# Kernel tuning notes

Hardware: AMD Instinct MI355X
Metric: run time of the kernel (lower is better)

## Reference

```python
import jax, jax.numpy as jnp
import numpy as np

B, S, DIM = 2, 2048, 2048
H, DH = 16, 128
FF = 4 * DIM
EPS = 1e-5


def layer_norm(x, w, b, eps=EPS):
    m = jnp.mean(x, axis=-1, keepdims=True)
    v = jnp.mean(jnp.square(x - m), axis=-1, keepdims=True)
    return (x - m) * jax.lax.rsqrt(v + eps) * w + b


def apply_rotary(x, cos, sin):
    # x: [B, H, S, DH]; cos/sin: [S, DH//2]; complex multiply on (even, odd) pairs
    x2 = x.reshape(*x.shape[:-1], DH // 2, 2)
    x0, x1 = x2[..., 0], x2[..., 1]
    c = cos[None, None, :, :]
    s = sin[None, None, :, :]
    r0 = x0 * c - x1 * s
    r1 = x0 * s + x1 * c
    return jnp.stack([r0, r1], axis=-1).reshape(x.shape)


def setup_inputs() -> dict:
    key = jax.random.key(0)
    ks = jax.random.split(key, 16)
    sc = 0.02
    pos = jnp.arange(S, dtype=jnp.float32)[:, None]
    inv_freq = 1.0 / (10000.0 ** (jnp.arange(0, DH // 2, dtype=jnp.float32) / (DH // 2)))
    ang = pos * inv_freq[None, :]
    return {
        "hidden_states": jax.random.normal(ks[0], (B, S, DIM), jnp.float32),
        "freqs_cos": jnp.cos(ang),
        "freqs_sin": jnp.sin(ang),
        "wq": jax.random.normal(ks[1], (DIM, H * DH), jnp.float32) * sc,
        "wk": jax.random.normal(ks[2], (DIM, H * DH), jnp.float32) * sc,
        "wv": jax.random.normal(ks[3], (DIM, H * DH), jnp.float32) * sc,
        "nq_w": jnp.ones((DH,), jnp.float32),
        "nq_b": jnp.zeros((DH,), jnp.float32),
        "nk_w": jnp.ones((DH,), jnp.float32),
        "nk_b": jnp.zeros((DH,), jnp.float32),
        "wo": jax.random.normal(ks[4], (H * DH, DIM), jnp.float32) * sc,
        "bo": jnp.zeros((DIM,), jnp.float32),
        "ln1_w": jnp.ones((DIM,), jnp.float32),
        "ln1_b": jnp.zeros((DIM,), jnp.float32),
        "ln3_w": jnp.ones((DIM,), jnp.float32),
        "ln3_b": jnp.zeros((DIM,), jnp.float32),
        "w1": jax.random.normal(ks[5], (DIM, FF), jnp.float32) * sc,
        "b1": jnp.zeros((FF,), jnp.float32),
        "w2": jax.random.normal(ks[6], (FF, DIM), jnp.float32) * sc,
        "b2": jnp.zeros((DIM,), jnp.float32),
    }


def reference(hidden_states, freqs_cos, freqs_sin, wq, wk, wv, nq_w, nq_b, nk_w, nk_b,
              wo, bo, ln1_w, ln1_b, ln3_w, ln3_b, w1, b1, w2, b2):
    x = hidden_states
    # --- self-attention branch ---
    n = layer_norm(x, ln1_w, ln1_b)                       # [B,S,DIM]
    q = (n @ wq).reshape(B, S, H, DH)
    k = (n @ wk).reshape(B, S, H, DH)
    v = (n @ wv).reshape(B, S, H, DH)
    # per-head QK LayerNorm (norm over dim_head)
    q = layer_norm(q, nq_w, nq_b)
    k = layer_norm(k, nk_w, nk_b)
    q = q.transpose(0, 2, 1, 3)                            # [B,H,S,DH]
    k = k.transpose(0, 2, 1, 3)
    v = v.transpose(0, 2, 1, 3)
    q = apply_rotary(q, freqs_cos, freqs_sin)
    k = apply_rotary(k, freqs_cos, freqs_sin)
    scale = DH ** -0.5
    scores = jnp.einsum("bhqd,bhkd->bhqk", q, k) * scale   # [B,H,S,S]
    probs = jax.nn.softmax(scores, axis=-1)
    attn = jnp.einsum("bhqk,bhkd->bhqd", probs, v)         # [B,H,S,DH]
    attn = attn.transpose(0, 2, 1, 3).reshape(B, S, H * DH)
    x = x + (attn @ wo + bo)
    # --- feed-forward branch ---
    n = layer_norm(x, ln3_w, ln3_b)
    h = jax.nn.gelu(n @ w1 + b1, approximate=False)
    x = x + (h @ w2 + b2)
    return x
```

## Files before the change

### kernel.cpp

```cpp
#include <hip/hip_runtime.h>
#include <hip/hip_bf16.h>
#include <stdint.h>

typedef __hip_bfloat16 bf16;
typedef float v4f __attribute__((ext_vector_type(4)));
typedef short v8s __attribute__((ext_vector_type(8)));

#define DEV __device__ __forceinline__

DEV float b2f(bf16 x) { return __bfloat162float(x); }
DEV bf16 f2b(float x) { return __float2bfloat16(x); }

DEV void load4(const float* p, float* f) {
  float4 t = *(const float4*)p;
  f[0] = t.x; f[1] = t.y; f[2] = t.z; f[3] = t.w;
}
DEV void load4(const bf16* p, float* f) {
  union { uint2 u; bf16 h[4]; } t;
  t.u = *(const uint2*)p;
#pragma unroll
  for (int i = 0; i < 4; i++) f[i] = b2f(t.h[i]);
}
DEV void load8(const float* p, float* f) {
  float4 a = ((const float4*)p)[0], b = ((const float4*)p)[1];
  f[0] = a.x; f[1] = a.y; f[2] = a.z; f[3] = a.w;
  f[4] = b.x; f[5] = b.y; f[6] = b.z; f[7] = b.w;
}
DEV void load8(const bf16* p, float* f) {
  union { uint4 u; bf16 h[8]; } t;
  t.u = *(const uint4*)p;
#pragma unroll
  for (int i = 0; i < 8; i++) f[i] = b2f(t.h[i]);
}
DEV void store4(bf16* p, const float* f) {
  union { uint2 u; bf16 h[4]; } t;
#pragma unroll
  for (int i = 0; i < 4; i++) t.h[i] = f2b(f[i]);
  *(uint2*)p = t.u;
}
DEV void store4(float* p, const float* f) {
  *(float4*)p = make_float4(f[0], f[1], f[2], f[3]);
}

DEV void gld_lds16(const bf16* g, bf16* l) {
  auto gp = reinterpret_cast<const __attribute__((address_space(1))) uint32_t*>(
      reinterpret_cast<uintptr_t>(g));
  auto lp = reinterpret_cast<__attribute__((address_space(3))) uint32_t*>(
      reinterpret_cast<uintptr_t>(l));
  __builtin_amdgcn_global_load_lds(gp, lp, 16, 0, 0);
}

template <typename XT>
__global__ __launch_bounds__(256)
void ln2048_kernel(const XT* __restrict__ x, const float* __restrict__ w,
                   const float* __restrict__ b, bf16* __restrict__ y) {
  const int N = 2048;
  int row = blockIdx.x, tid = threadIdx.x;
  const XT* xr = x + (size_t)row * N;
  bf16* yr = y + (size_t)row * N;
  float f[8], s = 0.f, ss = 0.f;
  load8(xr + tid * 8, f);
#pragma unroll
  for (int i = 0; i < 8; i++) { s += f[i]; ss += f[i] * f[i]; }
#pragma unroll
  for (int off = 32; off >= 1; off >>= 1) {
    s  += __shfl_xor(s, off, 64);
    ss += __shfl_xor(ss, off, 64);
  }
  __shared__ float red0[4], red1[4];
  int wv = tid >> 6;
  if ((tid & 63) == 0) { red0[wv] = s; red1[wv] = ss; }
  __syncthreads();
  s  = red0[0] + red0[1] + red0[2] + red0[3];
  ss = red1[0] + red1[1] + red1[2] + red1[3];
  float mean = s * (1.f / N);
  float var  = ss * (1.f / N) - mean * mean;
  float inv  = rsqrtf(var + 1e-5f);
  float wf[8], bf_[8];
  load8(w + tid * 8, wf);
  load8(b + tid * 8, bf_);
  union { uint4 u; bf16 h[8]; } vo;
#pragma unroll
  for (int i = 0; i < 8; i++)
    vo.h[i] = f2b((f[i] - mean) * inv * wf[i] + bf_[i]);
  ((uint4*)yr)[tid] = vo.u;
}

__global__ __launch_bounds__(256)
void headln_rope_kernel(bf16* __restrict__ q, const float* __restrict__ w,
                        const float* __restrict__ b, const float* __restrict__ fcos,
                        const float* __restrict__ fsin) {
  int tid = threadIdx.x;
  int wv = tid >> 6, ln = tid & 63;
  int idx = blockIdx.x * 4 + wv;
  int row = idx >> 4, h = idx & 15;
  int srow = row & 2047;
  bf16* p = q + (size_t)row * 2048 + h * 128 + ln * 2;
  union { unsigned int u; bf16 h2[2]; } v;
  v.u = *(const unsigned int*)p;
  float x0 = b2f(v.h2[0]), x1 = b2f(v.h2[1]);
  float s = x0 + x1, ss = x0 * x0 + x1 * x1;
#pragma unroll
  for (int off = 32; off >= 1; off >>= 1) {
    s  += __shfl_xor(s, off, 64);
    ss += __shfl_xor(ss, off, 64);
  }
  float mean = s * (1.f / 128.f);
  float var  = ss * (1.f / 128.f) - mean * mean;
  float inv  = rsqrtf(var + 1e-5f);
  float w0 = w[ln * 2], w1 = w[ln * 2 + 1];
  float b0 = b[ln * 2], b1 = b[ln * 2 + 1];
  x0 = (x0 - mean) * inv * w0 + b0;
  x1 = (x1 - mean) * inv * w1 + b1;
  float c  = fcos[srow * 64 + ln];
  float sn = fsin[srow * 64 + ln];
  v.h2[0] = f2b(x0 * c - x1 * sn);
  v.h2[1] = f2b(x0 * sn + x1 * c);
  *(unsigned int*)p = v.u;
}

__global__ __launch_bounds__(256)
void convT_kernel(const float* __restrict__ src, bf16* __restrict__ dst,
                  int K, int N) {
  __shared__ float T[64][65];
  int n0 = blockIdx.x * 64, k0 = blockIdx.y * 64;
  int t = threadIdx.x;
  int tr = t >> 4, tc4 = (t & 15) * 4;
#pragma unroll
  for (int it = 0; it < 4; it++) {
    float4 v = *(const float4*)&src[(size_t)(k0 + tr + 16 * it) * N + n0 + tc4];
    T[tr + 16 * it][tc4 + 0] = v.x;
    T[tr + 16 * it][tc4 + 1] = v.y;
    T[tr + 16 * it][tc4 + 2] = v.z;
    T[tr + 16 * it][tc4 + 3] = v.w;
  }
  __syncthreads();
#pragma unroll
  for (int it = 0; it < 4; it++) {
    int n = tr + 16 * it;
    union { uint2 u; bf16 h[4]; } o;
#pragma unroll
    for (int c = 0; c < 4; c++) o.h[c] = f2b(T[tc4 + c][n]);
    *(uint2*)&dst[(size_t)(n0 + n) * K + k0 + tc4] = o.u;
  }
}

template <int EPI, typename RT, typename OT>
__global__ __launch_bounds__(256, 2)
void mfma_gemm_kernel(const bf16* __restrict__ A, const bf16* __restrict__ BT,
                      OT* __restrict__ C, const float* __restrict__ bias,
                      const RT* __restrict__ res, int M, int N, int K) {
  __shared__ __align__(16) bf16 As[128 * 32];
  __shared__ __align__(16) bf16 Bs[128 * 32];
  int tid = threadIdx.x;
  int lane = tid & 63, wave = tid >> 6;
  int wr = wave >> 1, wc = wave & 1;
  int m0 = blockIdx.y * 128, n0 = blockIdx.x * 128;

  int ls_row = lane >> 2;
  int ls_k   = (lane & 3) * 8;
  int t0 = 2 * wave, t1 = 2 * wave + 1;
  const bf16* gA0 = A  + (size_t)(m0 + 16 * t0 + ls_row) * K + ls_k;
  const bf16* gA1 = A  + (size_t)(m0 + 16 * t1 + ls_row) * K + ls_k;
  const bf16* gB0 = BT + (size_t)(n0 + 16 * t0 + ls_row) * K + ls_k;
  const bf16* gB1 = BT + (size_t)(n0 + 16 * t1 + ls_row) * K + ls_k;
  bf16* lA0 = As + t0 * 512;
  bf16* lA1 = As + t1 * 512;
  bf16* lB0 = Bs + t0 * 512;
  bf16* lB1 = Bs + t1 * 512;

  int fr = lane & 15, fk = (lane >> 4) * 8;
  const bf16* pA = As + (wr * 64 + fr) * 32 + fk;
  const bf16* pB = Bs + (wc * 64 + fr) * 32 + fk;

  v4f acc[4][4];
#pragma unroll
  for (int i = 0; i < 4; i++)
#pragma unroll
    for (int j = 0; j < 4; j++) acc[i][j] = (v4f){0.f, 0.f, 0.f, 0.f};

  for (int k0 = 0; k0 < K; k0 += 32) {
    __syncthreads();
    gld_lds16(gA0, lA0); gld_lds16(gA1, lA1);
    gld_lds16(gB0, lB0); gld_lds16(gB1, lB1);
    gA0 += 32; gA1 += 32; gB0 += 32; gB1 += 32;
    __syncthreads();
    v8s af[4], bfr[4];
#pragma unroll
    for (int i = 0; i < 4; i++) af[i]  = *(const v8s*)(pA + i * 16 * 32);
#pragma unroll
    for (int j = 0; j < 4; j++) bfr[j] = *(const v8s*)(pB + j * 16 * 32);
#pragma unroll
    for (int i = 0; i < 4; i++)
#pragma unroll
      for (int j = 0; j < 4; j++)
        acc[i][j] = __builtin_amdgcn_mfma_f32_16x16x32_bf16(af[i], bfr[j],
                                                            acc[i][j], 0, 0, 0);
  }

  int rq = (lane >> 4) * 4;
#pragma unroll
  for (int j = 0; j < 4; j++) {
    int n = n0 + wc * 64 + j * 16 + (lane & 15);
    float bb = (EPI >= 1) ? bias[n] : 0.f;
#pragma unroll
    for (int i = 0; i < 4; i++) {
#pragma unroll
      for (int r = 0; r < 4; r++) {
        int m = m0 + wr * 64 + i * 16 + rq + r;
        float val = acc[i][j][r] + bb;
        if (EPI == 2)
          val = 0.5f * val * (1.f + erff(val * 0.70710678118654752f));
        if (EPI == 1) {
          if constexpr (__is_same(RT, float)) val += res[(size_t)m * N + n];
          else                                val += b2f(res[(size_t)m * N + n]);
        }
        if constexpr (__is_same(OT, float)) C[(size_t)m * N + n] = val;
        else                                C[(size_t)m * N + n] = f2b(val);
      }
    }
  }
}

template <int EPI, typename RT, typename OT>
__global__ __launch_bounds__(256)
void gemm_kernel(const bf16* __restrict__ A, const float* __restrict__ Bm,
                 OT* __restrict__ C, const float* __restrict__ bias,
                 const RT* __restrict__ res, int M, int N, int K) {
  const int BK = 32;
  __shared__ __align__(16) float As[BK][68];
  __shared__ __align__(16) float Bs[BK][68];
  int tid = threadIdx.x;
  int bm = blockIdx.y, bn = blockIdx.x;
  int tx = tid & 15, ty = tid >> 4;
  int am = tid >> 2, ak8 = (tid & 3) * 8;
  int bkr = tid >> 3, bn8 = (tid & 7) * 8;
  const bf16* Aptr = A + (size_t)(bm * 64 + am) * K + ak8;
  const float* Bptr = Bm + (size_t)bkr * N + bn * 64 + bn8;
  float acc[4][4] = {};
  for (int k0 = 0; k0 < K; k0 += BK) {
    float av[8], bv[8];
    load8(Aptr, av);
    load8(Bptr, bv);
    __syncthreads();
#pragma unroll
    for (int j = 0; j < 8; j++) As[ak8 + j][am] = av[j];
#pragma unroll
    for (int j = 0; j < 8; j++) Bs[bkr][bn8 + j] = bv[j];
    __syncthreads();
    Aptr += BK;
    Bptr += (size_t)BK * N;
#pragma unroll 8
    for (int kk = 0; kk < BK; kk++) {
      float a0[4], b0[4];
      *(float4*)a0 = *(const float4*)&As[kk][ty * 4];
      *(float4*)b0 = *(const float4*)&Bs[kk][tx * 4];
#pragma unroll
      for (int i = 0; i < 4; i++)
#pragma unroll
        for (int j = 0; j < 4; j++)
          acc[i][j] += a0[i] * b0[j];
    }
  }
  int m0 = bm * 64 + ty * 4, n0 = bn * 64 + tx * 4;
#pragma unroll
  for (int i = 0; i < 4; i++) {
    float r4[4];
#pragma unroll
    for (int j = 0; j < 4; j++) r4[j] = acc[i][j];
    if (EPI >= 1) {
      float bb[4];
      load4(bias + n0, bb);
#pragma unroll
      for (int j = 0; j < 4; j++) r4[j] += bb[j];
    }
    if (EPI == 2) {
#pragma unroll
      for (int j = 0; j < 4; j++)
        r4[j] = 0.5f * r4[j] * (1.f + erff(r4[j] * 0.70710678118654752f));
    }
    if (EPI == 1) {
      float rr[4];
      load4(res + (size_t)(m0 + i) * N + n0, rr);
#pragma unroll
      for (int j = 0; j < 4; j++) r4[j] += rr[j];
    }
    store4(&C[(size_t)(m0 + i) * N + n0], r4);
  }
}

#define VSWZ(r) (((((r) >> 3) ^ (r)) & 7) << 4)

__global__ __launch_bounds__(256, 2)
void attn_kernel(const bf16* __restrict__ q, const bf16* __restrict__ k,
                 const bf16* __restrict__ v, bf16* __restrict__ o) {
  const int S = 2048, HD = 2048;
  __shared__ __align__(16) char smem[57856];
  char* Ks0 = smem;
  char* Ks1 = smem + 16384;
  char* VtB = smem + 32768;
  char* PB  = smem + 49152;
  float* Lp = (float*)(smem + 57344);

  int id = blockIdx.x;
  int swzb = (id & 7) * 128 + (id >> 3);
  int bh = swzb >> 5, qb = swzb & 31;
  int q0 = qb * 64;
  size_t base = (size_t)(bh >> 4) * S * HD + (size_t)(bh & 15) * 128;

  int tid = threadIdx.x;
  int lane = tid & 63, wave = tid >> 6;
  int wr = wave >> 1, wc = wave & 1;
  int fr = lane & 15, fg = lane >> 4;

  if (tid < 128) Lp[tid] = 0.f;

  union V4U { uint4 u; bf16 h[8]; };
  int vr0 = (tid & 15) * 4, vd0 = (tid >> 4) * 8;

#pragma unroll
  for (int t = 0; t < 4; t++) {
    int ti = wave * 4 + t;
    int r = ti * 4 + fg;
    int cb = (fr * 16) ^ ((r & 7) << 4);
    gld_lds16(q + base + (size_t)(q0 + r) * HD + (cb >> 1), (bf16*)Ks0 + ti * 512);
    gld_lds16(k + base + (size_t)r * HD + (cb >> 1), (bf16*)Ks1 + ti * 512);
  }
  V4U vA[4], vB[4];
#pragma unroll
  for (int j = 0; j < 4; j++)
    vA[j].u = *(const uint4*)&v[base + (size_t)(vr0 + j) * HD + vd0];
  __syncthreads();

  v8s qfrag[2][4];
#pragma unroll
  for (int i = 0; i < 2; i++)
#pragma unroll
    for (int kk = 0; kk < 4; kk++) {
      int row = wr * 32 + i * 16 + fr;
      int off = row * 256 + ((kk * 64 + fg * 16) ^ ((row & 7) << 4));
      qfrag[i][kk] = *(const v8s*)(Ks0 + off);
    }
  __syncthreads();

  v4f oacc[2][4];
#pragma unroll
  for (int i = 0; i < 2; i++)
#pragma unroll
    for (int j = 0; j < 4; j++) oacc[i][j] = (v4f){0.f, 0.f, 0.f, 0.f};

  const float scale = 0.08838834764831845f;

#define ATTN_TILE(KT, KCUR, KNXT, VCUR, VNXT, STAGE_NEXT)                     \
  {                                                                           \
    _Pragma("unroll")                                                         \
    for (int c = 0; c < 8; c++) {                                             \
      int d = vd0 + c;                                                        \
      union { uint2 u2; bf16 hh[4]; } pk;                                     \
      _Pragma("unroll")                                                       \
      for (int j = 0; j < 4; j++) pk.hh[j] = VCUR[j].h[c];                    \
      *(uint2*)(VtB + d * 128 + ((vr0 * 2) ^ VSWZ(d))) = pk.u2;               \
    }                                                                         \
    if (STAGE_NEXT) {                                                         \
      _Pragma("unroll")                                                       \
      for (int t = 0; t < 4; t++) {                                           \
        int ti = wave * 4 + t;                                                \
        int r = ti * 4 + fg;                                                  \
        int cb = (fr * 16) ^ ((r & 7) << 4);                                  \
        gld_lds16(k + base + (size_t)((KT) + 64 + r) * HD + (cb >> 1),        \
                  (bf16*)(KNXT) + ti * 512);                                  \
      }                                                                       \
      _Pragma("unroll")                                                       \
      for (int j = 0; j < 4; j++)                                             \
        VNXT[j].u =                                                           \
            *(const uint4*)&v[base + (size_t)((KT) + 64 + vr0 + j) * HD + vd0]; \
    }                                                                         \
    v4f sacc[2][2];                                                           \
    _Pragma("unroll")                                                         \
    for (int i = 0; i < 2; i++)                                               \
      _Pragma("unroll")                                                       \
      for (int j = 0; j < 2; j++) sacc[i][j] = (v4f){0.f, 0.f, 0.f, 0.f};     \
    __builtin_amdgcn_s_setprio(1);                                            \
    _Pragma("unroll")                                                         \
    for (int kk = 0; kk < 4; kk++) {                                          \
      v8s kf[2];                                                              \
      _Pragma("unroll")                                                       \
      for (int j = 0; j < 2; j++) {                                           \
        int row = wc * 32 + j * 16 + fr;                                      \
        int off = row * 256 + ((kk * 64 + fg * 16) ^ ((row & 7) << 4));       \
        kf[j] = *(const v8s*)((KCUR) + off);                                  \
      }                                                                       \
      _Pragma("unroll")                                                       \
      for (int i = 0; i < 2; i++)                                             \
        _Pragma("unroll")                                                     \
        for (int j = 0; j < 2; j++)                                           \
          sacc[i][j] = __builtin_amdgcn_mfma_f32_16x16x32_bf16(               \
              qfrag[i][kk], kf[j], sacc[i][j], 0, 0, 0);                      \
    }                                                                         \
    __builtin_amdgcn_s_setprio(0);                                            \
    _Pragma("unroll")                                                         \
    for (int i = 0; i < 2; i++)                                               \
      _Pragma("unroll")                                                       \
      for (int r = 0; r < 4; r++) {                                           \
        int qrow = wr * 32 + i * 16 + fg * 4 + r;                             \
        float e0 = __expf(sacc[i][0][r] * scale);                             \
        float e1 = __expf(sacc[i][1][r] * scale);                             \
        int sw = VSWZ(qrow);                                                  \
        int c0 = wc * 64 + fr * 2;                                            \
        *(bf16*)(PB + qrow * 128 + (c0 ^ sw)) = f2b(e0);                      \
        *(bf16*)(PB + qrow * 128 + ((c0 + 32) ^ sw)) = f2b(e1);               \
        float s_ = e0 + e1;                                                   \
        s_ += __shfl_xor(s_, 1, 64);                                          \
        s_ += __shfl_xor(s_, 2, 64);                                          \
        s_ += __shfl_xor(s_, 4, 64);                                          \
        s_ += __shfl_xor(s_, 8, 64);                                          \
        if (fr == 0) Lp[wc * 64 + qrow] += s_;                                \
      }                                                                       \
    __syncthreads();                                                          \
    __builtin_amdgcn_s_setprio(1);                                            \
    _Pragma("unroll")                                                         \
    for (int kk2 = 0; kk2 < 2; kk2++) {                                       \
      v8s pf[2], vf[4];                                                       \
      _Pragma("unroll")                                                       \
      for (int i = 0; i < 2; i++) {                                           \
        int row = wr * 32 + i * 16 + fr;                                      \
        int off = row * 128 + ((kk2 * 64 + fg * 16) ^ VSWZ(row));             \
        pf[i] = *(const v8s*)(PB + off);                                      \
      }                                                                       \
      _Pragma("unroll")                                                       \
      for (int j = 0; j < 4; j++) {                                           \
        int row = wc * 64 + j * 16 + fr;                                      \
        int off = row * 128 + ((kk2 * 64 + fg * 16) ^ VSWZ(row));             \
        vf[j] = *(const v8s*)(VtB + off);                                     \
      }                                                                       \
      _Pragma("unroll")                                                       \
      for (int i = 0; i < 2; i++)                                             \
        _Pragma("unroll")                                                     \
        for (int j = 0; j < 4; j++)                                           \
          oacc[i][j] = __builtin_amdgcn_mfma_f32_16x16x32_bf16(               \
              pf[i], vf[j], oacc[i][j], 0, 0, 0);                             \
    }                                                                         \
    __builtin_amdgcn_s_setprio(0);                                            \
    __syncthreads();                                                          \
  }

  for (int tp = 0; tp < 16; tp++) {
    int kt = tp * 128;
    ATTN_TILE(kt, Ks1, Ks0, vA, vB, true);
    ATTN_TILE(kt + 64, Ks0, Ks1, vB, vA, (tp < 15));
  }
#undef ATTN_TILE

#pragma unroll
  for (int i = 0; i < 2; i++)
#pragma unroll
    for (int r = 0; r < 4; r++) {
      int qrow = wr * 32 + i * 16 + fg * 4 + r;
      float linv = 1.f / (Lp[qrow] + Lp[64 + qrow]);
#pragma unroll
      for (int j = 0; j < 4; j++) {
        int d = wc * 64 + j * 16 + fr;
        o[base + (size_t)(q0 + qrow) * HD + d] = f2b(oacc[i][j][r] * linv);
      }
    }
}

extern "C" void kernel_launch(void* const* d_in, const int* in_sizes, int n_in,
                              void* d_out, int out_size, void* d_ws, size_t ws_size,
                              hipStream_t stream) {
  (void)in_sizes; (void)n_in; (void)out_size;
  const float* x    = (const float*)d_in[0];
  const float* fcos = (const float*)d_in[1];
  const float* fsin = (const float*)d_in[2];
  const float* wq   = (const float*)d_in[3];
  const float* wk   = (const float*)d_in[4];
  const float* wv   = (const float*)d_in[5];
  const float* nqw  = (const float*)d_in[6];
  const float* nqb  = (const float*)d_in[7];
  const float* nkw  = (const float*)d_in[8];
  const float* nkb  = (const float*)d_in[9];
  const float* wo   = (const float*)d_in[10];
  const float* bo   = (const float*)d_in[11];
  const float* ln1w = (const float*)d_in[12];
  const float* ln1b = (const float*)d_in[13];
  const float* ln3w = (const float*)d_in[14];
  const float* ln3b = (const float*)d_in[15];
  const float* w1   = (const float*)d_in[16];
  const float* b1   = (const float*)d_in[17];
  const float* w2   = (const float*)d_in[18];
  const float* b2   = (const float*)d_in[19];
  float* out = (float*)d_out;

  const size_t SEG = (size_t)4096 * 2048;
  bf16* base = (bf16*)d_ws;
  bf16* q        = base + 0 * SEG;
  bf16* k        = base + 1 * SEG;
  bf16* v        = base + 2 * SEG;
  bf16* n1       = base + 3 * SEG;
  bf16* attn_out = base + 3 * SEG;
  bf16* x2       = base + 4 * SEG;
  bf16* n3       = base + 5 * SEG;
  bf16* h        = base + 0 * SEG;

  dim3 blk(256);
  ln2048_kernel<float><<<4096, blk, 0, stream>>>(x, ln1w, ln1b, n1);

  bool mfma_path = ws_size >= (size_t)128 * 1024 * 1024;
  if (mfma_path) {
    bf16* W = base + 6 * SEG;
    bf16* wqT = W;
    bf16* wkT = W + 4 * 1024 * 1024;
    bf16* wvT = W + 8 * 1024 * 1024;
    bf16* woT = W;
    bf16* w1T = W;
    bf16* w2T = W;

    dim3 cg22(32, 32);
    dim3 g16(16, 32);
    dim3 g64(64, 32);

    convT_kernel<<<cg22, blk, 0, stream>>>(wq, wqT, 2048, 2048);
    convT_kernel<<<cg22, blk, 0, stream>>>(wk, wkT, 2048, 2048);
    convT_kernel<<<cg22, blk, 0, stream>>>(wv, wvT, 2048, 2048);
    mfma_gemm_kernel<0, float, bf16><<<g16, blk, 0, stream>>>(n1, wqT, q, nullptr, nullptr, 4096, 2048, 2048);
    mfma_gemm_kernel<0, float, bf16><<<g16, blk, 0, stream>>>(n1, wkT, k, nullptr, nullptr, 4096, 2048, 2048);
    mfma_gemm_kernel<0, float, bf16><<<g16, blk, 0, stream>>>(n1, wvT, v, nullptr, nullptr, 4096, 2048, 2048);
    headln_rope_kernel<<<16384, blk, 0, stream>>>(q, nqw, nqb, fcos, fsin);
    headln_rope_kernel<<<16384, blk, 0, stream>>>(k, nkw, nkb, fcos, fsin);
    attn_kernel<<<1024, blk, 0, stream>>>(q, k, v, attn_out);
    convT_kernel<<<cg22, blk, 0, stream>>>(wo, woT, 2048, 2048);
    mfma_gemm_kernel<1, float, bf16><<<g16, blk, 0, stream>>>(attn_out, woT, x2, bo, x, 4096, 2048, 2048);
    ln2048_kernel<bf16><<<4096, blk, 0, stream>>>(x2, ln3w, ln3b, n3);
    convT_kernel<<<dim3(128, 32), blk, 0, stream>>>(w1, w1T, 2048, 8192);
    mfma_gemm_kernel<2, float, bf16><<<g64, blk, 0, stream>>>(n3, w1T, h, b1, nullptr, 4096, 8192, 2048);
    convT_kernel<<<dim3(32, 128), blk, 0, stream>>>(w2, w2T, 8192, 2048);
    mfma_gemm_kernel<1, bf16, float><<<g16, blk, 0, stream>>>(h, w2T, out, b2, x2, 4096, 2048, 8192);
  } else {
    dim3 g2048(32, 64), g8192(128, 64);
    gemm_kernel<0, float, bf16><<<g2048, blk, 0, stream>>>(n1, wq, q, nullptr, nullptr, 4096, 2048, 2048);
    gemm_kernel<0, float, bf16><<<g2048, blk, 0, stream>>>(n1, wk, k, nullptr, nullptr, 4096, 2048, 2048);
    gemm_kernel<0, float, bf16><<<g2048, blk, 0, stream>>>(n1, wv, v, nullptr, nullptr, 4096, 2048, 2048);
    headln_rope_kernel<<<16384, blk, 0, stream>>>(q, nqw, nqb, fcos, fsin);
    headln_rope_kernel<<<16384, blk, 0, stream>>>(k, nkw, nkb, fcos, fsin);
    attn_kernel<<<1024, blk, 0, stream>>>(q, k, v, attn_out);
    gemm_kernel<1, float, bf16><<<g2048, blk, 0, stream>>>(attn_out, wo, x2, bo, x, 4096, 2048, 2048);
    ln2048_kernel<bf16><<<4096, blk, 0, stream>>>(x2, ln3w, ln3b, n3);
    gemm_kernel<2, float, bf16><<<g8192, blk, 0, stream>>>(n3, w1, h, b1, nullptr, 4096, 8192, 2048);
    gemm_kernel<1, bf16, float><<<g2048, blk, 0, stream>>>(h, w2, out, b2, x2, 4096, 2048, 8192);
  }
}
```

Baseline: 1.026 ms.

## Fuse QKV GEMMs, swizzle GEMM block order, and enlarge attention query tile

Replaces the three Q/K/V projection GEMMs with one launch over a concatenated N=6144, scattering output columns into separate segments through a new ldc/segment-stride epilogue. This relies on wqT/wkT/wvT and q/k/v being laid out contiguously. Adds an XCD-aware block-index swizzle to the MFMA GEMM. Doubles the attention query tile from 64 to 128 rows per block, so K/V are loaded half as often, at the cost of more registers and more LDS.

```diff
diff --git a/kernel.cpp b/kernel.cpp
--- a/kernel.cpp
+++ b/kernel.cpp
@@ -149,13 +149,20 @@
 __global__ __launch_bounds__(256, 2)
 void mfma_gemm_kernel(const bf16* __restrict__ A, const bf16* __restrict__ BT,
                       OT* __restrict__ C, const float* __restrict__ bias,
-                      const RT* __restrict__ res, int M, int N, int K) {
+                      const RT* __restrict__ res, int M, int N, int K,
+                      int ldc_log2, size_t seg_stride) {
   __shared__ __align__(16) bf16 As[128 * 32];
   __shared__ __align__(16) bf16 Bs[128 * 32];
   int tid = threadIdx.x;
   int lane = tid & 63, wave = tid >> 6;
   int wr = wave >> 1, wc = wave & 1;
-  int m0 = blockIdx.y * 128, n0 = blockIdx.x * 128;
+
+  int nbx = gridDim.x;
+  int bid = blockIdx.y * nbx + blockIdx.x;
+  int nwg = nbx * gridDim.y;
+  int cpx = nwg >> 3;
+  int swz = (bid & 7) * cpx + (bid >> 3);
+  int m0 = (swz / nbx) * 128, n0 = (swz % nbx) * 128;
 
   int ls_row = lane >> 2;
   int ls_k   = (lane & 3) * 8;
@@ -199,10 +206,12 @@
   }
 
   int rq = (lane >> 4) * 4;
+  int ldm = 1 << ldc_log2;
 #pragma unroll
   for (int j = 0; j < 4; j++) {
     int n = n0 + wc * 64 + j * 16 + (lane & 15);
     float bb = (EPI >= 1) ? bias[n] : 0.f;
+    size_t cseg = (size_t)(n >> ldc_log2) * seg_stride + (n & (ldm - 1));
 #pragma unroll
     for (int i = 0; i < 4; i++) {
 #pragma unroll
@@ -215,8 +224,9 @@
           if constexpr (__is_same(RT, float)) val += res[(size_t)m * N + n];
           else                                val += b2f(res[(size_t)m * N + n]);
         }
-        if constexpr (__is_same(OT, float)) C[(size_t)m * N + n] = val;
-        else                                C[(size_t)m * N + n] = f2b(val);
+        size_t cix = cseg + ((size_t)m << ldc_log2);
+        if constexpr (__is_same(OT, float)) C[cix] = val;
+        else                                C[cix] = f2b(val);
       }
     }
   }
@@ -295,17 +305,17 @@
 void attn_kernel(const bf16* __restrict__ q, const bf16* __restrict__ k,
                  const bf16* __restrict__ v, bf16* __restrict__ o) {
   const int S = 2048, HD = 2048;
-  __shared__ __align__(16) char smem[57856];
+  __shared__ __align__(16) char smem[66560];
   char* Ks0 = smem;
   char* Ks1 = smem + 16384;
   char* VtB = smem + 32768;
   char* PB  = smem + 49152;
-  float* Lp = (float*)(smem + 57344);
+  float* Lp = (float*)(smem + 65536);
 
   int id = blockIdx.x;
-  int swzb = (id & 7) * 128 + (id >> 3);
-  int bh = swzb >> 5, qb = swzb & 31;
-  int q0 = qb * 64;
+  int swzb = (id & 7) * 64 + (id >> 3);
+  int bh = swzb >> 4, qb = swzb & 15;
+  int q0 = qb * 128;
   size_t base = (size_t)(bh >> 4) * S * HD + (size_t)(bh & 15) * 128;
 
   int tid = threadIdx.x;
@@ -313,39 +323,51 @@
   int wr = wave >> 1, wc = wave & 1;
   int fr = lane & 15, fg = lane >> 4;
 
-  if (tid < 128) Lp[tid] = 0.f;
+  Lp[tid] = 0.f;
 
   union V4U { uint4 u; bf16 h[8]; };
   int vr0 = (tid & 15) * 4, vd0 = (tid >> 4) * 8;
+
+#pragma unroll
+  for (int t = 0; t < 8; t++) {
+    int ti = wave * 8 + t;
+    int r = ti * 4 + fg;
+    int cb = (fr * 16) ^ ((r & 7) << 4);
+    bf16* dst = (bf16*)(ti < 16 ? Ks0 : Ks1) + (ti & 15) * 512;
+    gld_lds16(q + base + (size_t)(q0 + r) * HD + (cb >> 1), dst);
+  }
+  V4U vA[4], vB[4];
+#pragma unroll
+  for (int j = 0; j < 4; j++)
+    vA[j].u = *(const uint4*)&v[base + (size_t)(vr0 + j) * HD + vd0];
+  __syncthreads();
+
+  v8s qfrag[4][4];
+  {
+    const char* qbuf = wr ? Ks1 : Ks0;
+#pragma unroll
+    for (int i = 0; i < 4; i++)
+#pragma unroll
+      for (int kk = 0; kk < 4; kk++) {
+        int rb = i * 16 + fr;
+        int off = rb * 256 + ((kk * 64 + fg * 16) ^ ((rb & 7) << 4));
+        qfrag[i][kk] = *(const v8s*)(qbuf + off);
+      }
+  }
+  __syncthreads();
 
 #pragma unroll
   for (int t = 0; t < 4; t++) {
     int ti = wave * 4 + t;
     int r = ti * 4 + fg;
     int cb = (fr * 16) ^ ((r & 7) << 4);
-    gld_lds16(q + base + (size_t)(q0 + r) * HD + (cb >> 1), (bf16*)Ks0 + ti * 512);
-    gld_lds16(k + base + (size_t)r * HD + (cb >> 1), (bf16*)Ks1 + ti * 512);
-  }
-  V4U vA[4], vB[4];
-#pragma unroll
-  for (int j = 0; j < 4; j++)
-    vA[j].u = *(const uint4*)&v[base + (size_t)(vr0 + j) * HD + vd0];
+    gld_lds16(k + base + (size_t)r * HD + (cb >> 1), (bf16*)Ks0 + ti * 512);
+  }
   __syncthreads();
 
-  v8s qfrag[2][4];
-#pragma unroll
-  for (int i = 0; i < 2; i++)
-#pragma unroll
-    for (int kk = 0; kk < 4; kk++) {
-      int row = wr * 32 + i * 16 + fr;
-      int off = row * 256 + ((kk * 64 + fg * 16) ^ ((row & 7) << 4));
-      qfrag[i][kk] = *(const v8s*)(Ks0 + off);
-    }
-  __syncthreads();
-
-  v4f oacc[2][4];
-#pragma unroll
-  for (int i = 0; i < 2; i++)
+  v4f oacc[4][4];
+#pragma unroll
+  for (int i = 0; i < 4; i++)
 #pragma unroll
     for (int j = 0; j < 4; j++) oacc[i][j] = (v4f){0.f, 0.f, 0.f, 0.f};
 
@@ -375,9 +397,9 @@
         VNXT[j].u =                                                           \
             *(const uint4*)&v[base + (size_t)((KT) + 64 + vr0 + j) * HD + vd0]; \
     }                                                                         \
-    v4f sacc[2][2];                                                           \
+    v4f sacc[4][2];                                                           \
     _Pragma("unroll")                                                         \
-    for (int i = 0; i < 2; i++)                                               \
+    for (int i = 0; i < 4; i++)                                               \
       _Pragma("unroll")                                                       \
       for (int j = 0; j < 2; j++) sacc[i][j] = (v4f){0.f, 0.f, 0.f, 0.f};     \
     __builtin_amdgcn_s_setprio(1);                                            \
@@ -391,7 +413,7 @@
         kf[j] = *(const v8s*)((KCUR) + off);                                  \
       }                                                                       \
       _Pragma("unroll")                                                       \
-      for (int i = 0; i < 2; i++)                                             \
+      for (int i = 0; i < 4; i++)                                             \
         _Pragma("unroll")                                                     \
         for (int j = 0; j < 2; j++)                                           \
           sacc[i][j] = __builtin_amdgcn_mfma_f32_16x16x32_bf16(               \
@@ -399,10 +421,10 @@
     }                                                                         \
     __builtin_amdgcn_s_setprio(0);                                            \
     _Pragma("unroll")                                                         \
-    for (int i = 0; i < 2; i++)                                               \
+    for (int i = 0; i < 4; i++)                                               \
       _Pragma("unroll")                                                       \
       for (int r = 0; r < 4; r++) {                                           \
-        int qrow = wr * 32 + i * 16 + fg * 4 + r;                             \
+        int qrow = wr * 64 + i * 16 + fg * 4 + r;                             \
         float e0 = __expf(sacc[i][0][r] * scale);                             \
         float e1 = __expf(sacc[i][1][r] * scale);                             \
         int sw = VSWZ(qrow);                                                  \
@@ -414,16 +436,16 @@
         s_ += __shfl_xor(s_, 2, 64);                                          \
         s_ += __shfl_xor(s_, 4, 64);                                          \
         s_ += __shfl_xor(s_, 8, 64);                                          \
-        if (fr == 0) Lp[wc * 64 + qrow] += s_;                                \
+        if (fr == 0) Lp[wc * 128 + qrow] += s_;                               \
       }                                                                       \
     __syncthreads();                                                          \
     __builtin_amdgcn_s_setprio(1);                                            \
     _Pragma("unroll")                                                         \
     for (int kk2 = 0; kk2 < 2; kk2++) {                                       \
-      v8s pf[2], vf[4];                                                       \
-      _Pragma("unroll")                                                       \
-      for (int i = 0; i < 2; i++) {                                           \
-        int row = wr * 32 + i * 16 + fr;                                      \
+      v8s pf[4], vf[4];                                                       \
+      _Pragma("unroll")                                                       \
+      for (int i = 0; i < 4; i++) {                                           \
+        int row = wr * 64 + i * 16 + fr;                                      \
         int off = row * 128 + ((kk2 * 64 + fg * 16) ^ VSWZ(row));             \
         pf[i] = *(const v8s*)(PB + off);                                      \
       }                                                                       \
@@ -434,7 +456,7 @@
         vf[j] = *(const v8s*)(VtB + off);                                     \
       }                                                                       \
       _Pragma("unroll")                                                       \
-      for (int i = 0; i < 2; i++)                                             \
+      for (int i = 0; i < 4; i++)                                             \
         _Pragma("unroll")                                                     \
         for (int j = 0; j < 4; j++)                                           \
           oacc[i][j] = __builtin_amdgcn_mfma_f32_16x16x32_bf16(               \
@@ -446,17 +468,17 @@
 
   for (int tp = 0; tp < 16; tp++) {
     int kt = tp * 128;
-    ATTN_TILE(kt, Ks1, Ks0, vA, vB, true);
-    ATTN_TILE(kt + 64, Ks0, Ks1, vB, vA, (tp < 15));
+    ATTN_TILE(kt, Ks0, Ks1, vA, vB, true);
+    ATTN_TILE(kt + 64, Ks1, Ks0, vB, vA, (tp < 15));
   }
 #undef ATTN_TILE
 
 #pragma unroll
-  for (int i = 0; i < 2; i++)
+  for (int i = 0; i < 4; i++)
 #pragma unroll
     for (int r = 0; r < 4; r++) {
-      int qrow = wr * 32 + i * 16 + fg * 4 + r;
-      float linv = 1.f / (Lp[qrow] + Lp[64 + qrow]);
+      int qrow = wr * 64 + i * 16 + fg * 4 + r;
+      float linv = 1.f / (Lp[qrow] + Lp[128 + qrow]);
 #pragma unroll
       for (int j = 0; j < 4; j++) {
         int d = wc * 64 + j * 16 + fr;
@@ -517,24 +539,23 @@
 
     dim3 cg22(32, 32);
     dim3 g16(16, 32);
+    dim3 g48(48, 32);
     dim3 g64(64, 32);
 
     convT_kernel<<<cg22, blk, 0, stream>>>(wq, wqT, 2048, 2048);
     convT_kernel<<<cg22, blk, 0, stream>>>(wk, wkT, 2048, 2048);
     convT_kernel<<<cg22, blk, 0, stream>>>(wv, wvT, 2048, 2048);
-    mfma_gemm_kernel<0, float, bf16><<<g16, blk, 0, stream>>>(n1, wqT, q, nullptr, nullptr, 4096, 2048, 2048);
-    mfma_gemm_kernel<0, float, bf16><<<g16, blk, 0, stream>>>(n1, wkT, k, nullptr, nullptr, 4096, 2048, 2048);
-    mfma_gemm_kernel<0, float, bf16><<<g16, blk, 0, stream>>>(n1, wvT, v, nullptr, nullptr, 4096, 2048, 2048);
+    mfma_gemm_kernel<0, float, bf16><<<g48, blk, 0, stream>>>(n1, wqT, q, nullptr, nullptr, 4096, 6144, 2048, 11, SEG);
     headln_rope_kernel<<<16384, blk, 0, stream>>>(q, nqw, nqb, fcos, fsin);
     headln_rope_kernel<<<16384, blk, 0, stream>>>(k, nkw, nkb, fcos, fsin);
-    attn_kernel<<<1024, blk, 0, stream>>>(q, k, v, attn_out);
+    attn_kernel<<<512, blk, 0, stream>>>(q, k, v, attn_out);
     convT_kernel<<<cg22, blk, 0, stream>>>(wo, woT, 2048, 2048);
-    mfma_gemm_kernel<1, float, bf16><<<g16, blk, 0, stream>>>(attn_out, woT, x2, bo, x, 4096, 2048, 2048);
+    mfma_gemm_kernel<1, float, bf16><<<g16, blk, 0, stream>>>(attn_out, woT, x2, bo, x, 4096, 2048, 2048, 11, 0);
     ln2048_kernel<bf16><<<4096, blk, 0, stream>>>(x2, ln3w, ln3b, n3);
     convT_kernel<<<dim3(128, 32), blk, 0, stream>>>(w1, w1T, 2048, 8192);
-    mfma_gemm_kernel<2, float, bf16><<<g64, blk, 0, stream>>>(n3, w1T, h, b1, nullptr, 4096, 8192, 2048);
+    mfma_gemm_kernel<2, float, bf16><<<g64, blk, 0, stream>>>(n3, w1T, h, b1, nullptr, 4096, 8192, 2048, 13, 0);
     convT_kernel<<<dim3(32, 128), blk, 0, stream>>>(w2, w2T, 8192, 2048);
-    mfma_gemm_kernel<1, bf16, float><<<g16, blk, 0, stream>>>(h, w2T, out, b2, x2, 4096, 2048, 8192);
+    mfma_gemm_kernel<1, bf16, float><<<g16, blk, 0, stream>>>(h, w2T, out, b2, x2, 4096, 2048, 8192, 11, 0);
   } else {
     dim3 g2048(32, 64), g8192(128, 64);
     gemm_kernel<0, float, bf16><<<g2048, blk, 0, stream>>>(n1, wq, q, nullptr, nullptr, 4096, 2048, 2048);
@@ -542,7 +563,7 @@
     gemm_kernel<0, float, bf16><<<g2048, blk, 0, stream>>>(n1, wv, v, nullptr, nullptr, 4096, 2048, 2048);
     headln_rope_kernel<<<16384, blk, 0, stream>>>(q, nqw, nqb, fcos, fsin);
     headln_rope_kernel<<<16384, blk, 0, stream>>>(k, nkw, nkb, fcos, fsin);
-    attn_kernel<<<1024, blk, 0, stream>>>(q, k, v, attn_out);
+    attn_kernel<<<512, blk, 0, stream>>>(q, k, v, attn_out);
     gemm_kernel<1, float, bf16><<<g2048, blk, 0, stream>>>(attn_out, wo, x2, bo, x, 4096, 2048, 2048);
     ln2048_kernel<bf16><<<4096, blk, 0, stream>>>(x2, ln3w, ln3b, n3);
     gemm_kernel<2, float, bf16><<<g8192, blk, 0, stream>>>(n3, w1, h, b1, nullptr, 4096, 8192, 2048);
```

Result: slower. 1.125 ms (+9.7%).
